# Kernel optimization log

Hardware: AMD Instinct MI355X
Metric: run time of the kernel (lower is better)

Reference implementation:

```python
import jax, jax.numpy as jnp
import numpy as np

B, S, D = 4, 2048, 1024
NEG = -1e10

def setup_inputs() -> dict:
    key = jax.random.key(0)
    ks = jax.random.split(key, 10)
    inv = 1.0 / np.sqrt(D)
    return {
        "Q": jax.random.normal(ks[0], (B, S, D), dtype=jnp.float32),
        "K": jax.random.normal(ks[1], (B, S, D), dtype=jnp.float32),
        "V": jax.random.normal(ks[2], (B, S, D), dtype=jnp.float32),
        "attention_mask": jax.random.randint(ks[3], (B, 1, S), 0, 2, dtype=jnp.int32),
        "Wq": jax.random.uniform(ks[4], (D, D), jnp.float32, -inv, inv),
        "bq": jnp.zeros((D,), jnp.float32),
        "Wk": jax.random.uniform(ks[5], (D, D), jnp.float32, -inv, inv),
        "bk": jnp.zeros((D,), jnp.float32),
        "Wv": jax.random.uniform(ks[6], (D, D), jnp.float32, -inv, inv),
        "bv": jnp.zeros((D,), jnp.float32),
    }

def reference(Q, K, V, attention_mask, Wq, bq, Wk, bk, Wv, bv):
    # QKV projections (dropout is identity in eval mode)
    q = jnp.einsum('bsd,ed->bse', Q, Wq) + bq  # [B,S,D]
    k = jnp.einsum('bsd,ed->bse', K, Wk) + bk
    v = jnp.einsum('bsd,ed->bse', V, Wv) + bv
    scores = jnp.einsum('bqd,bkd->bqk', q, k) / jnp.sqrt(jnp.float32(D))  # [B,S,S]
    scores = jnp.where(attention_mask == 0, jnp.float32(NEG), scores)
    # additive causal mask: upper triangle (diag=1) gets NEG
    causal = jnp.triu(jnp.full((S, S), NEG, dtype=jnp.float32), k=1)
    scores = scores + causal
    attn = jax.nn.softmax(scores, axis=-1)
    return jnp.einsum('bqk,bkd->bqd', attn, v)
```

## Files before the change

kernel.cpp:

```cpp
#include <hip/hip_runtime.h>
#include <hip/hip_bf16.h>

typedef __bf16 bf16x8 __attribute__((ext_vector_type(8)));
typedef float floatx4 __attribute__((ext_vector_type(4)));
typedef unsigned short ushort_t;

__device__ __forceinline__ bf16x8 load8f(const float* p) {
  const float4* q = reinterpret_cast<const float4*>(p);
  float4 x = q[0], y = q[1];
  bf16x8 r;
  r[0] = (__bf16)x.x; r[1] = (__bf16)x.y; r[2] = (__bf16)x.z; r[3] = (__bf16)x.w;
  r[4] = (__bf16)y.x; r[5] = (__bf16)y.y; r[6] = (__bf16)y.z; r[7] = (__bf16)y.w;
  return r;
}

__device__ __forceinline__ void storeC(float* C, long idx, float v) { C[idx] = v; }
__device__ __forceinline__ void storeC(ushort_t* C, long idx, float v) {
  __bf16 b = (__bf16)v;
  C[idx] = __builtin_bit_cast(ushort_t, b);
}

__device__ __forceinline__ void glds16(const ushort_t* g, ushort_t* l) {
  __builtin_amdgcn_global_load_lds(
      (const __attribute__((address_space(1))) void*)g,
      (__attribute__((address_space(3))) void*)l, 16, 0, 0);
}

__global__ __launch_bounds__(256) void cvt3(
    const float* __restrict__ s0, const float* __restrict__ s1,
    const float* __restrict__ s2, ushort_t* __restrict__ dst, long n)
{
  const int z = blockIdx.y;
  const float* s = (z == 0) ? s0 : ((z == 1) ? s1 : s2);
  ushort_t* d = dst + (long)z * n;
  const long i = (((long)blockIdx.x * 256) + threadIdx.x) * 8;
  if (i < n) {
    bf16x8 v = load8f(s + i);
    *reinterpret_cast<bf16x8*>(d + i) = v;
  }
}

__global__ __launch_bounds__(256) void find_j0(
    const int* __restrict__ mask, int* __restrict__ j0, int S)
{
  const int b = blockIdx.x;
  const int* m = mask + (long)b * S;
  const int tid = threadIdx.x;
  int best = S;
  for (int j = tid; j < S; j += 256)
    if (m[j] != 0) best = min(best, j);
  #pragma unroll
  for (int off = 32; off; off >>= 1)
    best = min(best, __shfl_xor(best, off));
  __shared__ int red[4];
  if ((tid & 63) == 0) red[tid >> 6] = best;
  __syncthreads();
  if (tid == 0) j0[b] = min(min(red[0], red[1]), min(red[2], red[3]));
}

template<typename TC, int BIAS_MODE, bool CSKIP>
__global__ __launch_bounds__(256) void gemm_nt_bf16(
    const ushort_t* __restrict__ A, const ushort_t* __restrict__ B,
    const float* __restrict__ bias, const float* __restrict__ bias_b,
    TC* __restrict__ C, const int* __restrict__ j0p,
    int M, int N, int K, float alpha,
    long sAb, long sBb, long sCb)
{
  const int bz = blockIdx.z;
  const int bm = blockIdx.x, bn = blockIdx.y;

  if (CSKIP) {
    if (bn > bm && j0p[bz] <= bm * 128) return;
  }

  __shared__ ushort_t As[128 * 32];
  __shared__ ushort_t Bs[128 * 32];

  A += (long)bz * sAb;
  B += (long)bz * sBb;
  C += (long)bz * sCb;
  if (BIAS_MODE == 1 && bz == 1 && bias_b) bias = bias_b;

  const int tid = threadIdx.x;
  const int wave = tid >> 6, lane = tid & 63;
  const int wm = (wave & 1) * 64, wn = (wave >> 1) * 64;
  const int lr = lane & 15, lq = lane >> 4;

  const ushort_t* Ab = A + (long)(bm * 128) * K;
  const ushort_t* Bb = B + (long)(bn * 128) * K;

  const int seg0 = tid, seg1 = 256 + tid;
  const int sr0 = seg0 >> 2, sk0 = (seg0 & 3) << 3;
  const int sr1 = seg1 >> 2, sk1 = (seg1 & 3) << 3;

  floatx4 acc[4][4];
  #pragma unroll
  for (int i = 0; i < 4; ++i)
    #pragma unroll
    for (int j = 0; j < 4; ++j)
      acc[i][j] = (floatx4){0.f, 0.f, 0.f, 0.f};

  int aoff[4], boff[4];
  #pragma unroll
  for (int i = 0; i < 4; ++i) {
    aoff[i] = (wm + i * 16 + lr) * 32 + lq * 8;
    boff[i] = (wn + i * 16 + lr) * 32 + lq * 8;
  }

  const int ktiles = K >> 5;
  for (int kt = 0; kt < ktiles; ++kt) {
    const int kc = kt << 5;
    glds16(Ab + (long)sr0 * K + kc + sk0, &As[seg0 * 8]);
    glds16(Ab + (long)sr1 * K + kc + sk1, &As[seg1 * 8]);
    glds16(Bb + (long)sr0 * K + kc + sk0, &Bs[seg0 * 8]);
    glds16(Bb + (long)sr1 * K + kc + sk1, &Bs[seg1 * 8]);
    __syncthreads();

    bf16x8 af[4], bfr[4];
    #pragma unroll
    for (int i = 0; i < 4; ++i)
      af[i] = *reinterpret_cast<const bf16x8*>(&As[aoff[i]]);
    #pragma unroll
    for (int j = 0; j < 4; ++j)
      bfr[j] = *reinterpret_cast<const bf16x8*>(&Bs[boff[j]]);
    #pragma unroll
    for (int i = 0; i < 4; ++i)
      #pragma unroll
      for (int j = 0; j < 4; ++j)
        acc[i][j] = __builtin_amdgcn_mfma_f32_16x16x32_bf16(af[i], bfr[j], acc[i][j], 0, 0, 0);
    __syncthreads();
  }

  #pragma unroll
  for (int i = 0; i < 4; ++i) {
    #pragma unroll
    for (int j = 0; j < 4; ++j) {
      const int row0 = bm * 128 + wm + i * 16 + lq * 4;
      const int col  = bn * 128 + wn + j * 16 + lr;
      #pragma unroll
      for (int r = 0; r < 4; ++r) {
        float v = acc[i][j][r] * alpha;
        if (BIAS_MODE == 1) v += bias[col];
        if (BIAS_MODE == 2) v += bias[row0 + r];
        storeC(C, (long)(row0 + r) * N + col, v);
      }
    }
  }
}

__global__ __launch_bounds__(256) void softmax_causal(
    const ushort_t* __restrict__ Sc, ushort_t* __restrict__ P,
    const int* __restrict__ mask, int S)
{
  const int i = blockIdx.x, b = blockIdx.y;
  const ushort_t* row = Sc + ((long)b * S + i) * S;
  ushort_t* prow = P + ((long)b * S + i) * S;
  const int* mrow = mask + (long)b * S;
  const int tid = threadIdx.x;
  const int lane = tid & 63, wave = tid >> 6;
  const int j0 = tid * 8;
  __shared__ float red[4];

  bf16x8 sv = *reinterpret_cast<const bf16x8*>(row + j0);
  const int4* mp = reinterpret_cast<const int4*>(mrow + j0);
  int4 m0 = mp[0], m1 = mp[1];
  int mk[8] = {m0.x, m0.y, m0.z, m0.w, m1.x, m1.y, m1.z, m1.w};

  float vals[8];
  float mymax = -3.4e38f;
  #pragma unroll
  for (int u = 0; u < 8; ++u) {
    const int j = j0 + u;
    float v = (float)sv[u];
    if (mk[u] == 0) v = -1e10f;
    if (j > i) v += -1e10f;
    vals[u] = v;
    mymax = fmaxf(mymax, v);
  }
  #pragma unroll
  for (int off = 32; off; off >>= 1)
    mymax = fmaxf(mymax, __shfl_xor(mymax, off));
  if (lane == 0) red[wave] = mymax;
  __syncthreads();
  const float m = fmaxf(fmaxf(red[0], red[1]), fmaxf(red[2], red[3]));
  __syncthreads();

  float sum = 0.f;
  #pragma unroll
  for (int u = 0; u < 8; ++u) {
    const float e = __expf(vals[u] - m);
    vals[u] = e;
    sum += e;
  }
  #pragma unroll
  for (int off = 32; off; off >>= 1)
    sum += __shfl_xor(sum, off);
  if (lane == 0) red[wave] = sum;
  __syncthreads();
  const float tot = red[0] + red[1] + red[2] + red[3];
  const float inv = 1.0f / tot;

  bf16x8 pv;
  #pragma unroll
  for (int u = 0; u < 8; ++u) pv[u] = (__bf16)(vals[u] * inv);
  *reinterpret_cast<bf16x8*>(prow + j0) = pv;
}

extern "C" void kernel_launch(void* const* d_in, const int* in_sizes, int n_in,
                              void* d_out, int out_size, void* d_ws, size_t ws_size,
                              hipStream_t stream)
{
  const int B = 4, S = 2048, D = 1024;
  const float* Q  = (const float*)d_in[0];
  const float* K  = (const float*)d_in[1];
  const float* V  = (const float*)d_in[2];
  const int*   am = (const int*)d_in[3];
  const float* Wq = (const float*)d_in[4];
  const float* bq = (const float*)d_in[5];
  const float* Wk = (const float*)d_in[6];
  const float* bk = (const float*)d_in[7];
  const float* Wv = (const float*)d_in[8];
  const float* bv = (const float*)d_in[9];
  float* out = (float*)d_out;

  const long MS = (long)B * S;
  const long NQ = MS * D;
  const long NW = (long)D * D;
  const long NS = (long)B * S * S;

  ushort_t* qb = (ushort_t*)d_ws;
  ushort_t* kb = qb + NQ;
  ushort_t* vT = kb + NQ;
  ushort_t* Qb = vT + NQ;
  ushort_t* Wqb = Qb + 3 * NQ;
  int* j0 = (int*)(Wqb + 3 * NW);
  ushort_t* Sc = Qb;
  ushort_t* P  = qb;

  dim3 blk(256);

  cvt3<<<dim3((int)(NQ / 2048), 3), blk, 0, stream>>>(Q, K, V, Qb, NQ);
  cvt3<<<dim3((int)(NW / 2048), 3), blk, 0, stream>>>(Wq, Wk, Wv, Wqb, NW);
  find_j0<<<dim3(B), blk, 0, stream>>>(am, j0, S);

  gemm_nt_bf16<ushort_t, 1, false><<<dim3(64, 8, 2), blk, 0, stream>>>(
      Qb, Wqb, bq, bk, qb, nullptr, (int)MS, D, D, 1.0f, NQ, NW, NQ);
  gemm_nt_bf16<ushort_t, 2, false><<<dim3(8, 16, 4), blk, 0, stream>>>(
      Wqb + 2 * NW, Qb + 2 * NQ, bv, nullptr, vT, nullptr,
      D, S, D, 1.0f, 0L, (long)S * D, (long)D * S);

  gemm_nt_bf16<ushort_t, 0, true><<<dim3(16, 16, 4), blk, 0, stream>>>(
      qb, kb, nullptr, nullptr, Sc, j0, S, S, D, 0.03125f,
      (long)S * D, (long)S * D, (long)S * S);
  softmax_causal<<<dim3(S, B), blk, 0, stream>>>(Sc, P, am, S);
  gemm_nt_bf16<float, 0, false><<<dim3(16, 8, 4), blk, 0, stream>>>(
      P, vT, nullptr, nullptr, out, nullptr, S, D, S, 1.0f,
      (long)S * S, (long)D * S, (long)S * D);
}
```

Baseline: 376.5 us.

## Double-buffer GEMM LDS tiles and fold mask scan into conversion kernel

The bf16 GEMM now keeps two LDS buffers per operand. It prefetches the next K-tile with global_load_lds while computing on the current one, which drops one of the two barriers per K iteration. The separate find_j0 launch is merged into the first cvt3 kernel, removing one kernel launch. The cost is double the LDS footprint per block, which can lower occupancy. Overlap may also be limited if the compiler inserts a full vmcnt wait before the LDS reads.

```diff
diff --git a/kernel.cpp b/kernel.cpp
--- a/kernel.cpp
+++ b/kernel.cpp
@@ -28,7 +28,8 @@
 
 __global__ __launch_bounds__(256) void cvt3(
     const float* __restrict__ s0, const float* __restrict__ s1,
-    const float* __restrict__ s2, ushort_t* __restrict__ dst, long n)
+    const float* __restrict__ s2, ushort_t* __restrict__ dst, long n,
+    const int* __restrict__ mask, int* __restrict__ j0, int S, int B)
 {
   const int z = blockIdx.y;
   const float* s = (z == 0) ? s0 : ((z == 1) ? s1 : s2);
@@ -38,24 +39,21 @@
     bf16x8 v = load8f(s + i);
     *reinterpret_cast<bf16x8*>(d + i) = v;
   }
-}
-
-__global__ __launch_bounds__(256) void find_j0(
-    const int* __restrict__ mask, int* __restrict__ j0, int S)
-{
-  const int b = blockIdx.x;
-  const int* m = mask + (long)b * S;
-  const int tid = threadIdx.x;
-  int best = S;
-  for (int j = tid; j < S; j += 256)
-    if (m[j] != 0) best = min(best, j);
-  #pragma unroll
-  for (int off = 32; off; off >>= 1)
-    best = min(best, __shfl_xor(best, off));
-  __shared__ int red[4];
-  if ((tid & 63) == 0) red[tid >> 6] = best;
-  __syncthreads();
-  if (tid == 0) j0[b] = min(min(red[0], red[1]), min(red[2], red[3]));
+  if (mask && z == 0 && (int)blockIdx.x < B) {
+    const int b = blockIdx.x;
+    const int* m = mask + (long)b * S;
+    const int tid = threadIdx.x;
+    int best = S;
+    for (int j = tid; j < S; j += 256)
+      if (m[j] != 0) best = min(best, j);
+    #pragma unroll
+    for (int off = 32; off; off >>= 1)
+      best = min(best, __shfl_xor(best, off));
+    __shared__ int red[4];
+    if ((tid & 63) == 0) red[tid >> 6] = best;
+    __syncthreads();
+    if (tid == 0) j0[b] = min(min(red[0], red[1]), min(red[2], red[3]));
+  }
 }
 
 template<typename TC, int BIAS_MODE, bool CSKIP>
@@ -73,8 +71,8 @@
     if (bn > bm && j0p[bz] <= bm * 128) return;
   }
 
-  __shared__ ushort_t As[128 * 32];
-  __shared__ ushort_t Bs[128 * 32];
+  __shared__ ushort_t As[2][128 * 32];
+  __shared__ ushort_t Bs[2][128 * 32];
 
   A += (long)bz * sAb;
   B += (long)bz * sBb;
@@ -93,6 +91,12 @@
   const int sr0 = seg0 >> 2, sk0 = (seg0 & 3) << 3;
   const int sr1 = seg1 >> 2, sk1 = (seg1 & 3) << 3;
 
+  const ushort_t* a0 = Ab + (long)sr0 * K + sk0;
+  const ushort_t* a1 = Ab + (long)sr1 * K + sk1;
+  const ushort_t* b0 = Bb + (long)sr0 * K + sk0;
+  const ushort_t* b1 = Bb + (long)sr1 * K + sk1;
+  const int l0 = seg0 * 8, l1 = seg1 * 8;
+
   floatx4 acc[4][4];
   #pragma unroll
   for (int i = 0; i < 4; ++i)
@@ -107,28 +111,35 @@
     boff[i] = (wn + i * 16 + lr) * 32 + lq * 8;
   }
 
+  glds16(a0, &As[0][l0]);
+  glds16(a1, &As[0][l1]);
+  glds16(b0, &Bs[0][l0]);
+  glds16(b1, &Bs[0][l1]);
+
   const int ktiles = K >> 5;
   for (int kt = 0; kt < ktiles; ++kt) {
-    const int kc = kt << 5;
-    glds16(Ab + (long)sr0 * K + kc + sk0, &As[seg0 * 8]);
-    glds16(Ab + (long)sr1 * K + kc + sk1, &As[seg1 * 8]);
-    glds16(Bb + (long)sr0 * K + kc + sk0, &Bs[seg0 * 8]);
-    glds16(Bb + (long)sr1 * K + kc + sk1, &Bs[seg1 * 8]);
+    const int cur = kt & 1;
     __syncthreads();
-
+    if (kt + 1 < ktiles) {
+      const int kc = (kt + 1) << 5;
+      const int nxt = cur ^ 1;
+      glds16(a0 + kc, &As[nxt][l0]);
+      glds16(a1 + kc, &As[nxt][l1]);
+      glds16(b0 + kc, &Bs[nxt][l0]);
+      glds16(b1 + kc, &Bs[nxt][l1]);
+    }
     bf16x8 af[4], bfr[4];
     #pragma unroll
     for (int i = 0; i < 4; ++i)
-      af[i] = *reinterpret_cast<const bf16x8*>(&As[aoff[i]]);
+      af[i] = *reinterpret_cast<const bf16x8*>(&As[cur][aoff[i]]);
     #pragma unroll
     for (int j = 0; j < 4; ++j)
-      bfr[j] = *reinterpret_cast<const bf16x8*>(&Bs[boff[j]]);
+      bfr[j] = *reinterpret_cast<const bf16x8*>(&Bs[cur][boff[j]]);
     #pragma unroll
     for (int i = 0; i < 4; ++i)
       #pragma unroll
       for (int j = 0; j < 4; ++j)
         acc[i][j] = __builtin_amdgcn_mfma_f32_16x16x32_bf16(af[i], bfr[j], acc[i][j], 0, 0, 0);
-    __syncthreads();
   }
 
   #pragma unroll
@@ -226,7 +237,6 @@
   const long MS = (long)B * S;
   const long NQ = MS * D;
   const long NW = (long)D * D;
-  const long NS = (long)B * S * S;
 
   ushort_t* qb = (ushort_t*)d_ws;
   ushort_t* kb = qb + NQ;
@@ -239,9 +249,9 @@
 
   dim3 blk(256);
 
-  cvt3<<<dim3((int)(NQ / 2048), 3), blk, 0, stream>>>(Q, K, V, Qb, NQ);
-  cvt3<<<dim3((int)(NW / 2048), 3), blk, 0, stream>>>(Wq, Wk, Wv, Wqb, NW);
-  find_j0<<<dim3(B), blk, 0, stream>>>(am, j0, S);
+  cvt3<<<dim3((int)(NQ / 2048), 3), blk, 0, stream>>>(Q, K, V, Qb, NQ, am, j0, S, B);
+  cvt3<<<dim3((int)(NW / 2048), 3), blk, 0, stream>>>(Wq, Wk, Wv, Wqb, NW,
+                                                      nullptr, nullptr, S, B);
 
   gemm_nt_bf16<ushort_t, 1, false><<<dim3(64, 8, 2), blk, 0, stream>>>(
       Qb, Wqb, bq, bk, qb, nullptr, (int)MS, D, D, 1.0f, NQ, NW, NQ);
```

Measured after the change: 353.8 us. -6.0%, faster.
